# Kernel tuning notes

Hardware: AMD Instinct MI355X
Metric: run time of the kernel (lower is better)

The kernel has to match this reference:

```python
import itertools
import jax, jax.numpy as jnp
import numpy as np

B = 1024      # graphs
N = 40        # atoms per graph (module supports 1..49)
ETA = 64
K = 32        # num_clusters
ZD = 32       # z_dim
NA = 10       # num_atom_types
NB = 5        # num_bond_types + 1
CH, AH, BH = 128, 128, 64
TAU = 1.0


def _resblock(x, W1, b1, W2, b2, Ws, bs):
    # assumed ResidualBlock: Linear->ReLU->(dropout, eval=identity)->Linear + linear skip
    h = jax.nn.relu(x @ W1 + b1)
    return h @ W2 + b2 + (x @ Ws + bs)


def setup_inputs() -> dict:
    key = jax.random.key(0)
    ks = jax.random.split(key, 24)
    s = 0.05
    pairs = np.array(list(itertools.combinations(range(N), 2)), dtype=np.int32)  # [780,2]
    offsets = (np.arange(B, dtype=np.int32) * N)[:, None, None]
    edge_index = jnp.asarray((pairs[None] + offsets).reshape(-1, 2))  # [B*780, 2]
    return {
        "eta": jax.random.normal(ks[0], (B, ETA), jnp.float32),
        "gumbel_noise": jax.random.gumbel(ks[1], (B * N, K), jnp.float32),
        "z_noise": jax.random.normal(ks[2], (B * N, ZD), jnp.float32),
        "cW1": jax.random.normal(ks[3], (ETA, CH)) * s, "cb1": jnp.zeros((CH,)),
        "cW2": jax.random.normal(ks[4], (CH, K)) * s, "cb2": jnp.zeros((K,)),
        "cWs": jax.random.normal(ks[5], (ETA, K)) * s, "cbs": jnp.zeros((K,)),
        "cluster_means": jax.random.normal(ks[6], (K, ZD)),
        "cluster_log_sigmas": jnp.full((K, ZD), -2.0),
        "aW1": jax.random.normal(ks[7], (ZD, AH)) * s, "ab1": jnp.zeros((AH,)),
        "aW2": jax.random.normal(ks[8], (AH, NA)) * s, "ab2": jnp.zeros((NA,)),
        "aWs": jax.random.normal(ks[9], (ZD, NA)) * s, "abs_": jnp.zeros((NA,)),
        "bond_matrix": jax.random.normal(ks[10], (NB, ZD, ZD)),
        "bW1": jax.random.normal(ks[11], (NB, BH)) * s, "bb1": jnp.zeros((BH,)),
        "bW2": jax.random.normal(ks[12], (BH, NB)) * s, "bb2": jnp.zeros((NB,)),
        "bWs": jax.random.normal(ks[13], (NB, NB)) * s, "bbs": jnp.zeros((NB,)),
        "edge_index": edge_index,
    }


def reference(eta, gumbel_noise, z_noise,
              cW1, cb1, cW2, cb2, cWs, cbs,
              cluster_means, cluster_log_sigmas,
              aW1, ab1, aW2, ab2, aWs, abs_,
              bond_matrix, bW1, bb1, bW2, bb2, bWs, bbs,
              edge_index):
    # decode_eta: mixture weights
    pi = jax.nn.softmax(_resblock(eta, cW1, cb1, cW2, cb2, cWs, cbs), axis=1)  # [B,K]
    log_pi = jnp.log(pi)
    # sample_c: gumbel-softmax (hard, straight-through) per node
    logits = jnp.repeat(log_pi, N, axis=0)                      # [B*N, K]
    y_soft = jax.nn.softmax((logits + gumbel_noise) / TAU, axis=-1)
    y_hard = jax.nn.one_hot(jnp.argmax(y_soft, axis=-1), K, dtype=y_soft.dtype)
    c = y_hard + y_soft - jax.lax.stop_gradient(y_soft)         # straight-through
    # sample_z
    mu = c @ cluster_means                                      # [B*N, ZD]
    log_sigma = c @ cluster_log_sigmas
    sigma = jnp.exp(jnp.clip(log_sigma, -20.0, 30.0))
    z = z_noise * sigma + mu
    # decode_z: atom logits
    atom_types = _resblock(z, aW1, ab1, aW2, ab2, aWs, abs_)    # [B*N, NA]
    # symmetrized per-bond-type bilinear form over edge node pairs
    Wsym = 0.5 * (bond_matrix + jnp.swapaxes(bond_matrix, 1, 2))  # [NB, ZD, ZD]
    zi = z[edge_index[:, 0]]                                    # [E, ZD]
    zj = z[edge_index[:, 1]]                                    # [E, ZD]
    bil = jnp.einsum('ed,tdc,ec->et', zi, Wsym, zj)             # [E, NB]
    edge_logits = _resblock(bil, bW1, bb1, bW2, bb2, bWs, bbs)
    edge_types = jax.nn.softmax(edge_logits, axis=1)            # [E, NB]
    return atom_types, edge_types
```

## Files before the change

### kernel.cpp

```cpp
#include <hip/hip_runtime.h>

constexpr int NPAIR = 780;

constexpr int OFF_ZT = 0;
constexpr int OFF_A  = 1280;
constexpr int UTP    = 1280;
constexpr int OFF_BT = 5120;
constexpr int OFF_HW = 9020;
constexpr int SH_TOT = 9764;

__global__ __launch_bounds__(256) void prep_kernel(
    const float* __restrict__ eta,
    const float* __restrict__ cW1, const float* __restrict__ cb1,
    const float* __restrict__ cW2, const float* __restrict__ cb2,
    const float* __restrict__ cWs, const float* __restrict__ cbs,
    const float* __restrict__ bond, const float* __restrict__ lsig,
    const float* __restrict__ bW1, const float* __restrict__ bb1,
    const float* __restrict__ bW2, const float* __restrict__ bb2,
    const float* __restrict__ bWs, const float* __restrict__ bbs,
    float* __restrict__ log_pi, float* __restrict__ wsym,
    float* __restrict__ sigma, float* __restrict__ hwg)
{
  if (blockIdx.x < 256) {
    const int lane = threadIdx.x & 63, wid = threadIdx.x >> 6;
    const int row = blockIdx.x * 4 + wid;
    __shared__ __align__(16) float etas[4][64];
    __shared__ __align__(16) float hs[4][128];
    etas[wid][lane] = eta[row * 64 + lane];
    __syncthreads();
    float a0 = cb1[lane], a1 = cb1[lane + 64];
    for (int d = 0; d < 64; ++d) {
      float ed = etas[wid][d];
      a0 += ed * cW1[d * 128 + lane];
      a1 += ed * cW1[d * 128 + lane + 64];
    }
    hs[wid][lane] = fmaxf(a0, 0.f);
    hs[wid][lane + 64] = fmaxf(a1, 0.f);
    __syncthreads();
    if (lane < 32) {
      float x = cb2[lane] + cbs[lane];
      for (int j = 0; j < 128; ++j) x += hs[wid][j] * cW2[j * 32 + lane];
      for (int d = 0; d < 64; ++d) x += etas[wid][d] * cWs[d * 32 + lane];
      float m = x;
      for (int off = 16; off; off >>= 1) m = fmaxf(m, __shfl_xor(m, off));
      float e = __expf(x - m);
      float s = e;
      for (int off = 16; off; off >>= 1) s += __shfl_xor(s, off);
      log_pi[row * 32 + lane] = (x - m) - __logf(s);
    }
  } else {
    const int e = (blockIdx.x - 256) * 256 + threadIdx.x;
    if (e < 5120) {
      const int t = e >> 10, r = e & 1023, c = r >> 5, d = r & 31;
      wsym[e] = 0.5f * (bond[e] + bond[t * 1024 + d * 32 + c]);
    } else if (e < 6144) {
      const int q = e - 5120;
      sigma[q] = __expf(fminf(fmaxf(lsig[q], -20.f), 30.f));
    } else if (e < 6888) {
      const int idx = e - 6144;
      float v;
      if (idx < 320) v = bW1[idx];
      else if (idx < 384) v = bb1[idx - 320];
      else if (idx < 704) { int qq = idx - 384; int t2 = qq >> 6, j = qq & 63; v = bW2[j * 5 + t2]; }
      else if (idx < 709) v = bb2[idx - 704];
      else if (idx < 734) v = bWs[idx - 709];
      else v = bbs[idx - 734];
      hwg[idx] = v;
    }
  }
}

__global__ __launch_bounds__(256, 4) void fused_kernel(
    const float* __restrict__ log_pi, const float* __restrict__ gumbel,
    const float* __restrict__ z_noise,
    const float* __restrict__ means, const float* __restrict__ sigma,
    const float* __restrict__ aW1, const float* __restrict__ ab1,
    const float* __restrict__ aW2, const float* __restrict__ ab2,
    const float* __restrict__ aWs, const float* __restrict__ abs_,
    const float* __restrict__ wsym, const float* __restrict__ hwg,
    float* __restrict__ atom_out, float* __restrict__ edge_out)
{
  __shared__ __align__(16) float S[SH_TOT];
  const int tid = threadIdx.x;
  const int m = blockIdx.x;

  if (tid < 40) {
    const int n = m * 40 + tid;
    float lp[32];
    #pragma unroll
    for (int c = 0; c < 32; ++c) lp[c] = log_pi[m * 32 + c];
    float g[32];
    const float4* g4 = (const float4*)(gumbel + (size_t)n * 32);
    #pragma unroll
    for (int q = 0; q < 8; ++q) {
      float4 v = g4[q];
      g[4*q] = v.x; g[4*q+1] = v.y; g[4*q+2] = v.z; g[4*q+3] = v.w;
    }
    int kb = 0; float vb = lp[0] + g[0];
    #pragma unroll
    for (int c = 1; c < 32; ++c) {
      float v = lp[c] + g[c];
      if (v > vb) { vb = v; kb = c; }
    }
    const float4* zn4 = (const float4*)(z_noise + (size_t)n * 32);
    const float4* mk4 = (const float4*)(means + kb * 32);
    const float4* sg4 = (const float4*)(sigma + kb * 32);
    #pragma unroll
    for (int q = 0; q < 8; ++q) {
      float4 zn = zn4[q], mk = mk4[q], sg = sg4[q];
      S[OFF_ZT + (4*q    ) * 40 + tid] = zn.x * sg.x + mk.x;
      S[OFF_ZT + (4*q + 1) * 40 + tid] = zn.y * sg.y + mk.y;
      S[OFF_ZT + (4*q + 2) * 40 + tid] = zn.z * sg.z + mk.z;
      S[OFF_ZT + (4*q + 3) * 40 + tid] = zn.w * sg.w + mk.w;
    }
  } else if (tid >= 64) {
    for (int idx = tid - 64; idx < 744; idx += 192) S[OFF_HW + idx] = hwg[idx];
  }
  __syncthreads();

  for (int u = tid; u < 320; u += 256) {
    const int ng = u >> 5, jg = u & 31;
    const int n0 = ng * 4, j0 = jg * 4;
    float acc[4][4];
    #pragma unroll
    for (int a = 0; a < 4; ++a)
      #pragma unroll
      for (int b = 0; b < 4; ++b) acc[a][b] = 0.f;
    #pragma unroll 8
    for (int c = 0; c < 32; ++c) {
      float4 zv = *(const float4*)&S[OFF_ZT + c * 40 + n0];
      float4 wv = *(const float4*)(aW1 + c * 128 + j0);
      acc[0][0] += zv.x * wv.x; acc[0][1] += zv.x * wv.y; acc[0][2] += zv.x * wv.z; acc[0][3] += zv.x * wv.w;
      acc[1][0] += zv.y * wv.x; acc[1][1] += zv.y * wv.y; acc[1][2] += zv.y * wv.z; acc[1][3] += zv.y * wv.w;
      acc[2][0] += zv.z * wv.x; acc[2][1] += zv.z * wv.y; acc[2][2] += zv.z * wv.z; acc[2][3] += zv.z * wv.w;
      acc[3][0] += zv.w * wv.x; acc[3][1] += zv.w * wv.y; acc[3][2] += zv.w * wv.z; acc[3][3] += zv.w * wv.w;
    }
    float4 bv = *(const float4*)(ab1 + j0);
    float bj[4] = {bv.x, bv.y, bv.z, bv.w};
    #pragma unroll
    for (int b = 0; b < 4; ++b) {
      float4 hv;
      hv.x = fmaxf(acc[0][b] + bj[b], 0.f);
      hv.y = fmaxf(acc[1][b] + bj[b], 0.f);
      hv.z = fmaxf(acc[2][b] + bj[b], 0.f);
      hv.w = fmaxf(acc[3][b] + bj[b], 0.f);
      *(float4*)&S[OFF_A + (j0 + b) * 44 + n0] = hv;
    }
  }
  __syncthreads();

  if (tid < 200) {
    const int n = tid / 5, kp = tid - (tid / 5) * 5, k0 = kp * 2;
    float a0 = ab2[k0] + abs_[k0];
    float a1 = ab2[k0 + 1] + abs_[k0 + 1];
    #pragma unroll 8
    for (int c = 0; c < 32; ++c) {
      float zc = S[OFF_ZT + c * 40 + n];
      float2 w = *(const float2*)(aWs + c * 10 + k0);
      a0 += zc * w.x; a1 += zc * w.y;
    }
    #pragma unroll 8
    for (int j = 0; j < 128; ++j) {
      float hv = S[OFF_A + j * 44 + n];
      float2 w = *(const float2*)(aW2 + j * 10 + k0);
      a0 += hv * w.x; a1 += hv * w.y;
    }
    *(float2*)(atom_out + (size_t)m * 400 + n * 10 + k0) = make_float2(a0, a1);
  }
  __syncthreads();

  #pragma unroll
  for (int R = 0; R < 2; ++R) {
    const int tbase = (R == 0) ? 0 : 3;
    const int nplanes = (R == 0) ? 3 : 2;
    for (int u = tid; u < nplanes * 80; u += 256) {
      const int tl = u / 80, r = u - tl * 80;
      const int dg = r / 10, ig = r - dg * 10;
      const int d0 = dg * 4, i0 = ig * 4;
      const float* wg = wsym + (tbase + tl) * 1024;
      float acc[4][4];
      #pragma unroll
      for (int a = 0; a < 4; ++a)
        #pragma unroll
        for (int b = 0; b < 4; ++b) acc[a][b] = 0.f;
      #pragma unroll 8
      for (int c = 0; c < 32; ++c) {
        float4 zv = *(const float4*)&S[OFF_ZT + c * 40 + i0];
        float4 wv = *(const float4*)(wg + c * 32 + d0);
        acc[0][0] += wv.x * zv.x; acc[0][1] += wv.x * zv.y; acc[0][2] += wv.x * zv.z; acc[0][3] += wv.x * zv.w;
        acc[1][0] += wv.y * zv.x; acc[1][1] += wv.y * zv.y; acc[1][2] += wv.y * zv.z; acc[1][3] += wv.y * zv.w;
        acc[2][0] += wv.z * zv.x; acc[2][1] += wv.z * zv.y; acc[2][2] += wv.z * zv.z; acc[2][3] += wv.z * zv.w;
        acc[3][0] += wv.w * zv.x; acc[3][1] += wv.w * zv.y; acc[3][2] += wv.w * zv.z; acc[3][3] += wv.w * zv.w;
      }
      #pragma unroll
      for (int a = 0; a < 4; ++a)
        *(float4*)&S[OFF_A + tl * UTP + (d0 + a) * 40 + i0] =
            make_float4(acc[a][0], acc[a][1], acc[a][2], acc[a][3]);
    }
    __syncthreads();

    if (tid < nplanes * 55) {
      const int tl = tid / 55;
      int q = tid - tl * 55;
      int ig = 0;
      while (q >= 10 - ig) { q -= 10 - ig; ++ig; }
      const int jg = ig + q;
      const int i0 = ig * 4, j0 = jg * 4;
      float acc[4][4];
      #pragma unroll
      for (int a = 0; a < 4; ++a)
        #pragma unroll
        for (int b = 0; b < 4; ++b) acc[a][b] = 0.f;
      #pragma unroll 8
      for (int d = 0; d < 32; ++d) {
        float4 uv = *(const float4*)&S[OFF_A + tl * UTP + d * 40 + i0];
        float4 zv = *(const float4*)&S[OFF_ZT + d * 40 + j0];
        acc[0][0] += uv.x * zv.x; acc[0][1] += uv.x * zv.y; acc[0][2] += uv.x * zv.z; acc[0][3] += uv.x * zv.w;
        acc[1][0] += uv.y * zv.x; acc[1][1] += uv.y * zv.y; acc[1][2] += uv.y * zv.z; acc[1][3] += uv.y * zv.w;
        acc[2][0] += uv.z * zv.x; acc[2][1] += uv.z * zv.y; acc[2][2] += uv.z * zv.z; acc[2][3] += uv.z * zv.w;
        acc[3][0] += uv.w * zv.x; acc[3][1] += uv.w * zv.y; acc[3][2] += uv.w * zv.z; acc[3][3] += uv.w * zv.w;
      }
      const int tg = tbase + tl;
      #pragma unroll
      for (int a = 0; a < 4; ++a) {
        const int i = i0 + a;
        #pragma unroll
        for (int b = 0; b < 4; ++b) {
          const int j = j0 + b;
          if (i < j) {
            const int p = i * (79 - i) / 2 + (j - i - 1);
            S[OFF_BT + tg * 780 + p] = acc[a][b];
          }
        }
      }
    }
    __syncthreads();
  }

  const float* w1h = &S[OFF_HW];
  const float* b1h = &S[OFF_HW + 320];
  const float* w2t = &S[OFF_HW + 384];
  const float* b2h = &S[OFF_HW + 704];
  const float* wsh = &S[OFF_HW + 709];
  const float* bsh = &S[OFF_HW + 734];

  float bil5[3][5], lg[3][5];
  #pragma unroll
  for (int s = 0; s < 3; ++s) {
    const int p = tid + (s << 8);
    #pragma unroll
    for (int t = 0; t < 5; ++t) bil5[s][t] = S[OFF_BT + t * 780 + p];
    #pragma unroll
    for (int t2 = 0; t2 < 5; ++t2) {
      float a = b2h[t2] + bsh[t2];
      #pragma unroll
      for (int t = 0; t < 5; ++t) a += bil5[s][t] * wsh[t * 5 + t2];
      lg[s][t2] = a;
    }
  }
  for (int j4 = 0; j4 < 16; ++j4) {
    float4 bb = ((const float4*)b1h)[j4];
    float4 h[3];
    #pragma unroll
    for (int s = 0; s < 3; ++s) h[s] = bb;
    #pragma unroll
    for (int t = 0; t < 5; ++t) {
      float4 w1 = ((const float4*)(w1h + t * 64))[j4];
      #pragma unroll
      for (int s = 0; s < 3; ++s) {
        float bt = bil5[s][t];
        h[s].x += bt * w1.x; h[s].y += bt * w1.y; h[s].z += bt * w1.z; h[s].w += bt * w1.w;
      }
    }
    #pragma unroll
    for (int s = 0; s < 3; ++s) {
      h[s].x = fmaxf(h[s].x, 0.f); h[s].y = fmaxf(h[s].y, 0.f);
      h[s].z = fmaxf(h[s].z, 0.f); h[s].w = fmaxf(h[s].w, 0.f);
    }
    #pragma unroll
    for (int t2 = 0; t2 < 5; ++t2) {
      float4 w2 = ((const float4*)(w2t + t2 * 64))[j4];
      #pragma unroll
      for (int s = 0; s < 3; ++s)
        lg[s][t2] += h[s].x * w2.x + h[s].y * w2.y + h[s].z * w2.z + h[s].w * w2.w;
    }
  }
  #pragma unroll
  for (int s = 0; s < 3; ++s) {
    const int p = tid + (s << 8);
    float mx = lg[s][0];
    #pragma unroll
    for (int t2 = 1; t2 < 5; ++t2) mx = fmaxf(mx, lg[s][t2]);
    float e[5], sum = 0.f;
    #pragma unroll
    for (int t2 = 0; t2 < 5; ++t2) { e[t2] = __expf(lg[s][t2] - mx); sum += e[t2]; }
    float inv = 1.f / sum;
    float* outp = edge_out + ((size_t)m * NPAIR + p) * 5;
    #pragma unroll
    for (int t2 = 0; t2 < 5; ++t2) outp[t2] = e[t2] * inv;
  }

  if (tid < 12) {
    const int p = 768 + tid;
    float bt[5], lgt[5];
    #pragma unroll
    for (int t = 0; t < 5; ++t) bt[t] = S[OFF_BT + t * 780 + p];
    #pragma unroll
    for (int t2 = 0; t2 < 5; ++t2) {
      float a = b2h[t2] + bsh[t2];
      #pragma unroll
      for (int t = 0; t < 5; ++t) a += bt[t] * wsh[t * 5 + t2];
      lgt[t2] = a;
    }
    for (int j = 0; j < 64; ++j) {
      float hv = b1h[j];
      #pragma unroll
      for (int t = 0; t < 5; ++t) hv += bt[t] * w1h[t * 64 + j];
      hv = fmaxf(hv, 0.f);
      #pragma unroll
      for (int t2 = 0; t2 < 5; ++t2) lgt[t2] += hv * w2t[t2 * 64 + j];
    }
    float mx = lgt[0];
    #pragma unroll
    for (int t2 = 1; t2 < 5; ++t2) mx = fmaxf(mx, lgt[t2]);
    float e[5], sum = 0.f;
    #pragma unroll
    for (int t2 = 0; t2 < 5; ++t2) { e[t2] = __expf(lgt[t2] - mx); sum += e[t2]; }
    float inv = 1.f / sum;
    float* outp = edge_out + ((size_t)m * NPAIR + p) * 5;
    #pragma unroll
    for (int t2 = 0; t2 < 5; ++t2) outp[t2] = e[t2] * inv;
  }
}

extern "C" void kernel_launch(void* const* d_in, const int* in_sizes, int n_in,
                              void* d_out, int out_size, void* d_ws, size_t ws_size,
                              hipStream_t stream) {
  const float* eta    = (const float*)d_in[0];
  const float* gumbel = (const float*)d_in[1];
  const float* z_noise= (const float*)d_in[2];
  const float* cW1 = (const float*)d_in[3];
  const float* cb1 = (const float*)d_in[4];
  const float* cW2 = (const float*)d_in[5];
  const float* cb2 = (const float*)d_in[6];
  const float* cWs = (const float*)d_in[7];
  const float* cbs = (const float*)d_in[8];
  const float* means = (const float*)d_in[9];
  const float* lsig  = (const float*)d_in[10];
  const float* aW1 = (const float*)d_in[11];
  const float* ab1 = (const float*)d_in[12];
  const float* aW2 = (const float*)d_in[13];
  const float* ab2 = (const float*)d_in[14];
  const float* aWs = (const float*)d_in[15];
  const float* abs_= (const float*)d_in[16];
  const float* bond= (const float*)d_in[17];
  const float* bW1 = (const float*)d_in[18];
  const float* bb1 = (const float*)d_in[19];
  const float* bW2 = (const float*)d_in[20];
  const float* bb2 = (const float*)d_in[21];
  const float* bWs = (const float*)d_in[22];
  const float* bbs = (const float*)d_in[23];

  float* wsym   = (float*)d_ws;
  float* sigma  = wsym + 5120;
  float* hwg    = sigma + 1024;
  float* log_pi = hwg + 768;
  float* atom_out = (float*)d_out;
  float* edge_out = atom_out + (size_t)1024 * 400;

  prep_kernel<<<284, 256, 0, stream>>>(eta, cW1, cb1, cW2, cb2, cWs, cbs,
                                       bond, lsig, bW1, bb1, bW2, bb2, bWs, bbs,
                                       log_pi, wsym, sigma, hwg);
  fused_kernel<<<1024, 256, 0, stream>>>(log_pi, gumbel, z_noise,
                                         means, sigma, aW1, ab1, aW2, ab2, aWs, abs_,
                                         wsym, hwg, atom_out, edge_out);
}
```

Baseline: 189.9 us.

## Use 512-thread blocks so each stage runs in one pass

Doubles the fused kernel block size to 512 threads. The atom hidden-layer GEMM and bilinear plane GEMMs now finish in a single pass instead of striding loops. The edge MLP handles at most two pairs per thread, which removes the separate 12-thread tail path. The ReLU hidden activations are stored node-major with padded stride 132, changing the shared-memory access pattern for the second atom layer. The risks are register pressure from launch_bounds(512,8) and fewer resident blocks per CU.

```diff
diff --git a/kernel.cpp b/kernel.cpp
--- a/kernel.cpp
+++ b/kernel.cpp
@@ -1,6 +1,7 @@
 #include <hip/hip_runtime.h>
 
 constexpr int NPAIR = 780;
+constexpr int BD = 512;
 
 constexpr int OFF_ZT = 0;
 constexpr int OFF_A  = 1280;
@@ -70,7 +71,7 @@
   }
 }
 
-__global__ __launch_bounds__(256, 4) void fused_kernel(
+__global__ __launch_bounds__(BD, 8) void fused_kernel(
     const float* __restrict__ log_pi, const float* __restrict__ gumbel,
     const float* __restrict__ z_noise,
     const float* __restrict__ means, const float* __restrict__ sigma,
@@ -114,12 +115,12 @@
       S[OFF_ZT + (4*q + 3) * 40 + tid] = zn.w * sg.w + mk.w;
     }
   } else if (tid >= 64) {
-    for (int idx = tid - 64; idx < 744; idx += 192) S[OFF_HW + idx] = hwg[idx];
+    for (int idx = tid - 64; idx < 744; idx += (BD - 64)) S[OFF_HW + idx] = hwg[idx];
   }
   __syncthreads();
 
-  for (int u = tid; u < 320; u += 256) {
-    const int ng = u >> 5, jg = u & 31;
+  if (tid < 320) {
+    const int ng = tid >> 5, jg = tid & 31;
     const int n0 = ng * 4, j0 = jg * 4;
     float acc[4][4];
     #pragma unroll
@@ -136,15 +137,14 @@
       acc[3][0] += zv.w * wv.x; acc[3][1] += zv.w * wv.y; acc[3][2] += zv.w * wv.z; acc[3][3] += zv.w * wv.w;
     }
     float4 bv = *(const float4*)(ab1 + j0);
-    float bj[4] = {bv.x, bv.y, bv.z, bv.w};
-    #pragma unroll
-    for (int b = 0; b < 4; ++b) {
+    #pragma unroll
+    for (int a = 0; a < 4; ++a) {
       float4 hv;
-      hv.x = fmaxf(acc[0][b] + bj[b], 0.f);
-      hv.y = fmaxf(acc[1][b] + bj[b], 0.f);
-      hv.z = fmaxf(acc[2][b] + bj[b], 0.f);
-      hv.w = fmaxf(acc[3][b] + bj[b], 0.f);
-      *(float4*)&S[OFF_A + (j0 + b) * 44 + n0] = hv;
+      hv.x = fmaxf(acc[a][0] + bv.x, 0.f);
+      hv.y = fmaxf(acc[a][1] + bv.y, 0.f);
+      hv.z = fmaxf(acc[a][2] + bv.z, 0.f);
+      hv.w = fmaxf(acc[a][3] + bv.w, 0.f);
+      *(float4*)&S[OFF_A + (n0 + a) * 132 + j0] = hv;
     }
   }
   __syncthreads();
@@ -161,7 +161,7 @@
     }
     #pragma unroll 8
     for (int j = 0; j < 128; ++j) {
-      float hv = S[OFF_A + j * 44 + n];
+      float hv = S[OFF_A + n * 132 + j];
       float2 w = *(const float2*)(aW2 + j * 10 + k0);
       a0 += hv * w.x; a1 += hv * w.y;
     }
@@ -173,8 +173,8 @@
   for (int R = 0; R < 2; ++R) {
     const int tbase = (R == 0) ? 0 : 3;
     const int nplanes = (R == 0) ? 3 : 2;
-    for (int u = tid; u < nplanes * 80; u += 256) {
-      const int tl = u / 80, r = u - tl * 80;
+    if (tid < nplanes * 80) {
+      const int tl = tid / 80, r = tid - tl * 80;
       const int dg = r / 10, ig = r - dg * 10;
       const int d0 = dg * 4, i0 = ig * 4;
       const float* wg = wsym + (tbase + tl) * 1024;
@@ -244,12 +244,15 @@
   const float* wsh = &S[OFF_HW + 709];
   const float* bsh = &S[OFF_HW + 734];
 
-  float bil5[3][5], lg[3][5];
+  const int p1 = BD + tid;
+  const bool v1 = (p1 < NPAIR);
+  const int pc[2] = { tid, v1 ? p1 : 0 };
+
+  float bil5[2][5], lg[2][5];
   #pragma unroll
-  for (int s = 0; s < 3; ++s) {
-    const int p = tid + (s << 8);
-    #pragma unroll
-    for (int t = 0; t < 5; ++t) bil5[s][t] = S[OFF_BT + t * 780 + p];
+  for (int s = 0; s < 2; ++s) {
+    #pragma unroll
+    for (int t = 0; t < 5; ++t) bil5[s][t] = S[OFF_BT + t * 780 + pc[s]];
     #pragma unroll
     for (int t2 = 0; t2 < 5; ++t2) {
       float a = b2h[t2] + bsh[t2];
@@ -260,20 +263,19 @@
   }
   for (int j4 = 0; j4 < 16; ++j4) {
     float4 bb = ((const float4*)b1h)[j4];
-    float4 h[3];
-    #pragma unroll
-    for (int s = 0; s < 3; ++s) h[s] = bb;
+    float4 h[2];
+    h[0] = bb; h[1] = bb;
     #pragma unroll
     for (int t = 0; t < 5; ++t) {
       float4 w1 = ((const float4*)(w1h + t * 64))[j4];
       #pragma unroll
-      for (int s = 0; s < 3; ++s) {
+      for (int s = 0; s < 2; ++s) {
         float bt = bil5[s][t];
         h[s].x += bt * w1.x; h[s].y += bt * w1.y; h[s].z += bt * w1.z; h[s].w += bt * w1.w;
       }
     }
     #pragma unroll
-    for (int s = 0; s < 3; ++s) {
+    for (int s = 0; s < 2; ++s) {
       h[s].x = fmaxf(h[s].x, 0.f); h[s].y = fmaxf(h[s].y, 0.f);
       h[s].z = fmaxf(h[s].z, 0.f); h[s].w = fmaxf(h[s].w, 0.f);
     }
@@ -281,13 +283,13 @@
     for (int t2 = 0; t2 < 5; ++t2) {
       float4 w2 = ((const float4*)(w2t + t2 * 64))[j4];
       #pragma unroll
-      for (int s = 0; s < 3; ++s)
+      for (int s = 0; s < 2; ++s)
         lg[s][t2] += h[s].x * w2.x + h[s].y * w2.y + h[s].z * w2.z + h[s].w * w2.w;
     }
   }
   #pragma unroll
-  for (int s = 0; s < 3; ++s) {
-    const int p = tid + (s << 8);
+  for (int s = 0; s < 2; ++s) {
+    if (s == 1 && !v1) continue;
     float mx = lg[s][0];
     #pragma unroll
     for (int t2 = 1; t2 < 5; ++t2) mx = fmaxf(mx, lg[s][t2]);
@@ -295,39 +297,7 @@
     #pragma unroll
     for (int t2 = 0; t2 < 5; ++t2) { e[t2] = __expf(lg[s][t2] - mx); sum += e[t2]; }
     float inv = 1.f / sum;
-    float* outp = edge_out + ((size_t)m * NPAIR + p) * 5;
-    #pragma unroll
-    for (int t2 = 0; t2 < 5; ++t2) outp[t2] = e[t2] * inv;
-  }
-
-  if (tid < 12) {
-    const int p = 768 + tid;
-    float bt[5], lgt[5];
-    #pragma unroll
-    for (int t = 0; t < 5; ++t) bt[t] = S[OFF_BT + t * 780 + p];
-    #pragma unroll
-    for (int t2 = 0; t2 < 5; ++t2) {
-      float a = b2h[t2] + bsh[t2];
-      #pragma unroll
-      for (int t = 0; t < 5; ++t) a += bt[t] * wsh[t * 5 + t2];
-      lgt[t2] = a;
-    }
-    for (int j = 0; j < 64; ++j) {
-      float hv = b1h[j];
-      #pragma unroll
-      for (int t = 0; t < 5; ++t) hv += bt[t] * w1h[t * 64 + j];
-      hv = fmaxf(hv, 0.f);
-      #pragma unroll
-      for (int t2 = 0; t2 < 5; ++t2) lgt[t2] += hv * w2t[t2 * 64 + j];
-    }
-    float mx = lgt[0];
-    #pragma unroll
-    for (int t2 = 1; t2 < 5; ++t2) mx = fmaxf(mx, lgt[t2]);
-    float e[5], sum = 0.f;
-    #pragma unroll
-    for (int t2 = 0; t2 < 5; ++t2) { e[t2] = __expf(lgt[t2] - mx); sum += e[t2]; }
-    float inv = 1.f / sum;
-    float* outp = edge_out + ((size_t)m * NPAIR + p) * 5;
+    float* outp = edge_out + ((size_t)m * NPAIR + pc[s]) * 5;
     #pragma unroll
     for (int t2 = 0; t2 < 5; ++t2) outp[t2] = e[t2] * inv;
   }
@@ -371,7 +341,7 @@
   prep_kernel<<<284, 256, 0, stream>>>(eta, cW1, cb1, cW2, cb2, cWs, cbs,
                                        bond, lsig, bW1, bb1, bW2, bb2, bWs, bbs,
                                        log_pi, wsym, sigma, hwg);
-  fused_kernel<<<1024, 256, 0, stream>>>(log_pi, gumbel, z_noise,
-                                         means, sigma, aW1, ab1, aW2, ab2, aWs, abs_,
-                                         wsym, hwg, atom_out, edge_out);
+  fused_kernel<<<1024, BD, 0, stream>>>(log_pi, gumbel, z_noise,
+                                        means, sigma, aW1, ab1, aW2, ab2, aWs, abs_,
+                                        wsym, hwg, atom_out, edge_out);
 }
```

Measured after the change: 203.9 us. 7.4% more time.

## Read edge MLP weights from global, transpose hidden layout, simplify bilinear loop

Applied to the files above, without the earlier changes.

Stops staging the 744-float edge-MLP weight block in shared memory and reads those weights directly from global memory (hwg), which shrinks shared usage and removes a copy loop. The atom hidden activations are stored row-major per atom (stride 132) instead of per hidden unit, so the second atom layer reads contiguous values per thread. The bilinear plane loop becomes a single guarded iteration because the work count never exceeds the thread count. The global weight reads are uniform across threads and rely on scalar or cache loads; the new hidden layout may alter LDS bank conflicts.

```diff
diff --git a/kernel.cpp b/kernel.cpp
--- a/kernel.cpp
+++ b/kernel.cpp
@@ -6,8 +6,7 @@
 constexpr int OFF_A  = 1280;
 constexpr int UTP    = 1280;
 constexpr int OFF_BT = 5120;
-constexpr int OFF_HW = 9020;
-constexpr int SH_TOT = 9764;
+constexpr int SH_TOT = 9020;
 
 __global__ __launch_bounds__(256) void prep_kernel(
     const float* __restrict__ eta,
@@ -113,8 +112,6 @@
       S[OFF_ZT + (4*q + 2) * 40 + tid] = zn.z * sg.z + mk.z;
       S[OFF_ZT + (4*q + 3) * 40 + tid] = zn.w * sg.w + mk.w;
     }
-  } else if (tid >= 64) {
-    for (int idx = tid - 64; idx < 744; idx += 192) S[OFF_HW + idx] = hwg[idx];
   }
   __syncthreads();
 
@@ -136,15 +133,14 @@
       acc[3][0] += zv.w * wv.x; acc[3][1] += zv.w * wv.y; acc[3][2] += zv.w * wv.z; acc[3][3] += zv.w * wv.w;
     }
     float4 bv = *(const float4*)(ab1 + j0);
-    float bj[4] = {bv.x, bv.y, bv.z, bv.w};
-    #pragma unroll
-    for (int b = 0; b < 4; ++b) {
+    #pragma unroll
+    for (int a = 0; a < 4; ++a) {
       float4 hv;
-      hv.x = fmaxf(acc[0][b] + bj[b], 0.f);
-      hv.y = fmaxf(acc[1][b] + bj[b], 0.f);
-      hv.z = fmaxf(acc[2][b] + bj[b], 0.f);
-      hv.w = fmaxf(acc[3][b] + bj[b], 0.f);
-      *(float4*)&S[OFF_A + (j0 + b) * 44 + n0] = hv;
+      hv.x = fmaxf(acc[a][0] + bv.x, 0.f);
+      hv.y = fmaxf(acc[a][1] + bv.y, 0.f);
+      hv.z = fmaxf(acc[a][2] + bv.z, 0.f);
+      hv.w = fmaxf(acc[a][3] + bv.w, 0.f);
+      *(float4*)&S[OFF_A + (n0 + a) * 132 + j0] = hv;
     }
   }
   __syncthreads();
@@ -161,7 +157,7 @@
     }
     #pragma unroll 8
     for (int j = 0; j < 128; ++j) {
-      float hv = S[OFF_A + j * 44 + n];
+      float hv = S[OFF_A + n * 132 + j];
       float2 w = *(const float2*)(aW2 + j * 10 + k0);
       a0 += hv * w.x; a1 += hv * w.y;
     }
@@ -173,8 +169,8 @@
   for (int R = 0; R < 2; ++R) {
     const int tbase = (R == 0) ? 0 : 3;
     const int nplanes = (R == 0) ? 3 : 2;
-    for (int u = tid; u < nplanes * 80; u += 256) {
-      const int tl = u / 80, r = u - tl * 80;
+    if (tid < nplanes * 80) {
+      const int tl = tid / 80, r = tid - tl * 80;
       const int dg = r / 10, ig = r - dg * 10;
       const int d0 = dg * 4, i0 = ig * 4;
       const float* wg = wsym + (tbase + tl) * 1024;
@@ -237,12 +233,12 @@
     __syncthreads();
   }
 
-  const float* w1h = &S[OFF_HW];
-  const float* b1h = &S[OFF_HW + 320];
-  const float* w2t = &S[OFF_HW + 384];
-  const float* b2h = &S[OFF_HW + 704];
-  const float* wsh = &S[OFF_HW + 709];
-  const float* bsh = &S[OFF_HW + 734];
+  const float* w1h = hwg;
+  const float* b1h = hwg + 320;
+  const float* w2t = hwg + 384;
+  const float* b2h = hwg + 704;
+  const float* wsh = hwg + 709;
+  const float* bsh = hwg + 734;
 
   float bil5[3][5], lg[3][5];
   #pragma unroll
```

New measurement: 183.0 us. 1.04x faster.
